# Kernel tuning notes

Hardware: AMD Instinct MI355X
Metric: run time of the kernel (lower is better)

## Reference

```python
import jax, jax.numpy as jnp
import numpy as np

L, H, D_IN, D_OUT = 2, 768, 768, 512


def _gru_layer(x, w_ih, w_hh, b_ih, b_hh):
    # x: [B,T,D]; w_ih: [3H,D]; w_hh: [3H,H]; b_ih,b_hh: [3H]
    # PyTorch GRU gate order: r, z, n
    gates_x = jnp.einsum('btd,gd->btg', x, w_ih) + b_ih  # [B,T,3H], precomputed once
    gates_x = jnp.swapaxes(gates_x, 0, 1)  # [T,B,3H] for scan over time
    h0 = jnp.zeros((x.shape[0], w_hh.shape[1]), dtype=x.dtype)

    def step(h, gx):
        gh = h @ w_hh.T + b_hh  # [B,3H]
        xr, xz, xn = jnp.split(gx, 3, axis=-1)
        hr, hz, hn = jnp.split(gh, 3, axis=-1)
        r = jax.nn.sigmoid(xr + hr)
        z = jax.nn.sigmoid(xz + hz)
        n = jnp.tanh(xn + r * hn)
        h_new = (1.0 - z) * n + z * h
        return h_new, h_new

    _, ys = jax.lax.scan(step, h0, gates_x)  # ys: [T,B,H]
    return jnp.swapaxes(ys, 0, 1)  # [B,T,H]


def setup_inputs() -> dict:
    key = jax.random.key(0)
    ks = jax.random.split(key, 6)
    B, T = 16, 1024
    s = 1.0 / np.sqrt(H)  # PyTorch RNN init scale
    x = jax.random.normal(ks[0], (B, T, D_IN), dtype=jnp.float32)
    # stacked per-layer GRU weights (D_IN == H so layer 0 stacks cleanly)
    w_ih = jax.random.uniform(ks[1], (L, 3 * H, H), minval=-s, maxval=s, dtype=jnp.float32)
    w_hh = jax.random.uniform(ks[2], (L, 3 * H, H), minval=-s, maxval=s, dtype=jnp.float32)
    b_ih = jax.random.uniform(ks[3], (L, 3 * H), minval=-s, maxval=s, dtype=jnp.float32)
    b_hh = jax.random.uniform(ks[4], (L, 3 * H), minval=-s, maxval=s, dtype=jnp.float32)
    w_fc = jax.random.normal(ks[5], (D_OUT, H), dtype=jnp.float32) * 0.02
    b_fc = jnp.zeros((D_OUT,), dtype=jnp.float32)
    return {"x": x, "w_ih": w_ih, "w_hh": w_hh, "b_ih": b_ih, "b_hh": b_hh,
            "w_fc": w_fc, "b_fc": b_fc}


def reference(x, w_ih, w_hh, b_ih, b_hh, w_fc, b_fc):
    out = x
    for l in range(L):  # small fixed layer loop
        out = _gru_layer(out, w_ih[l], w_hh[l], b_ih[l], b_hh[l])
    out = jnp.einsum('bth,oh->bto', out, w_fc) + b_fc  # Linear(768->512)
    return jax.nn.gelu(out, approximate=False)  # torch gelu (exact)
```

## Files before the change

kernel.cpp:

```cpp
#include <hip/hip_runtime.h>
#include <hip/hip_bf16.h>

#define H     768
#define G3    2304
#define BATCH 16
#define TLEN  1024
#define DOUT  512
#define SLICE 32
#define WPG   24
#define NSCAN 96
#define NFC   64
#define NWG   160
#define NTHR  384

typedef __attribute__((ext_vector_type(8))) short short8;
typedef __attribute__((ext_vector_type(4))) float f32x4;
typedef __attribute__((ext_vector_type(4))) unsigned int u32x4;

union U8 { short8 s; unsigned u[4]; unsigned long long q[2]; };

__device__ __forceinline__ float b2f(ushort u) {
  union { unsigned int ui; float f; } v; v.ui = ((unsigned int)u) << 16; return v.f;
}
__device__ __forceinline__ ushort f2b(float f) {
  union { float f; unsigned int ui; } v; v.f = f;
  unsigned int u = v.ui;
  return (ushort)((u + 0x7fffu + ((u >> 16) & 1u)) >> 16);
}

__device__ __forceinline__ unsigned long long agent_ld64(const void* p) {
  return __hip_atomic_load((const unsigned long long*)p, __ATOMIC_RELAXED, __HIP_MEMORY_SCOPE_AGENT);
}
__device__ __forceinline__ unsigned agent_ld32(const void* p) {
  return __hip_atomic_load((const unsigned*)p, __ATOMIC_RELAXED, __HIP_MEMORY_SCOPE_AGENT);
}
__device__ __forceinline__ void agent_st32(void* p, unsigned v) {
  __hip_atomic_store((unsigned*)p, v, __ATOMIC_RELAXED, __HIP_MEMORY_SCOPE_AGENT);
}
__device__ __forceinline__ void agent_st64(void* p, unsigned long long v) {
  __hip_atomic_store((unsigned long long*)p, v, __ATOMIC_RELAXED, __HIP_MEMORY_SCOPE_AGENT);
}

__device__ __forceinline__ void ld64B_agent(const void* p, u32x4* r) {
  asm volatile(
    "global_load_dwordx4 %0, %4, off sc0 sc1\n\t"
    "global_load_dwordx4 %1, %4, off offset:16 sc0 sc1\n\t"
    "global_load_dwordx4 %2, %4, off offset:32 sc0 sc1\n\t"
    "global_load_dwordx4 %3, %4, off offset:48 sc0 sc1\n\t"
    "s_waitcnt vmcnt(0)"
    : "=&v"(r[0]), "=&v"(r[1]), "=&v"(r[2]), "=&v"(r[3])
    : "v"(p) : "memory");
}

__device__ __forceinline__ short8 loadA8(const void* base, bool bf, size_t eidx) {
  if (bf) return *(const short8*)((const ushort*)base + eidx);
  const uint4* f = (const uint4*)((const float*)base + eidx);
  uint4 lo = f[0];
  uint4 hi = f[1];
  U8 r;
  r.u[0] = __builtin_amdgcn_perm(lo.y, lo.x, 0x07060302);
  r.u[1] = __builtin_amdgcn_perm(lo.w, lo.z, 0x07060302);
  r.u[2] = __builtin_amdgcn_perm(hi.y, hi.x, 0x07060302);
  r.u[3] = __builtin_amdgcn_perm(hi.w, hi.z, 0x07060302);
  return r.s;
}
__device__ __forceinline__ short8 loadW8(const void* base, bool bf, size_t eidx) {
  if (bf) return *(const short8*)((const ushort*)base + eidx);
  const float* f = (const float*)base + eidx;
  short8 r;
  #pragma unroll
  for (int i = 0; i < 8; i++) r[i] = (short)f2b(f[i]);
  return r;
}
__device__ __forceinline__ float loadS(const void* p, bool bf, size_t i) {
  return bf ? b2f(((const ushort*)p)[i]) : ((const float*)p)[i];
}

__device__ __forceinline__ bool detect_bf16(const unsigned* xw, int tid, int nthr, int* sh) {
  if (tid == 0) *sh = 0;
  __syncthreads();
  int c = 0;
  for (int i = tid; i < 4096; i += nthr) {
    int e = (int)((xw[i] >> 7) & 0xFF);
    c += (e >= 110 && e <= 140) ? 1 : 0;
  }
  atomicAdd(sh, c);
  __syncthreads();
  return *sh > 2048;
}

__device__ __forceinline__ unsigned* flagp(unsigned* flags, int grp, int wgi, int rep) {
  return flags + (((grp * WPG + wgi) * 4 + rep) * 32);
}

__global__ __launch_bounds__(NTHR) void scan_kernel(
    const void* __restrict__ x,
    const void* __restrict__ w_ih,
    const void* __restrict__ w_hh,
    const void* __restrict__ b_ih,
    const void* __restrict__ b_hh,
    const void* __restrict__ w_fc,
    const void* __restrict__ b_fc,
    unsigned int* flags,
    ushort* h1buf,
    float*  gxbuf1,
    float*  gxbuf2,
    ushort* y2,
    void* __restrict__ out)
{
  const int wg   = blockIdx.x;
  const int tid  = threadIdx.x;
  const int wave = tid >> 6;
  const int lane = tid & 63;
  const int quad = lane >> 4;

  __shared__ ushort h_lds[BATCH * H];
  __shared__ float ghs[96 * 17];
  __shared__ float hold[BATCH * SLICE];
  __shared__ float bih_s[96], bhh_s[96];
  __shared__ int   detsh;

  const bool isbf = detect_bf16((const unsigned*)x, tid, NTHR, &detsh);

  if (wg >= NSCAN) {
    const int fcw = wg - NSCAN;
    const unsigned* fpoll = (wave == 0 && lane < WPG)
        ? flagp(flags, 3, lane, (fcw < 32) ? 2 : 3) : nullptr;
    const int sb  = tid / 24;
    const int seg = tid % 24;
    const int sx  = sb & 7;
    const int ar  = lane & 15;
    const int arx = ar & 7;

    for (int i = 0; i < 16; i++) {
      const int t = fcw + 64 * i;
      if (wave == 0) {
        const int tgt = t + 5;
        for (;;) {
          int v = fpoll ? (int)agent_ld32(fpoll) : 0x7FFFFFFF;
          if (__ballot(v < tgt) == 0ull) break;
          __builtin_amdgcn_s_sleep(8);
        }
      }
      __syncthreads();

      {
        const ushort* src = y2 + ((size_t)sb * TLEN + t) * H + seg * 32;
        u32x4 r4[4];
        ld64B_agent(src, r4);
        #pragma unroll
        for (int j = 0; j < 4; j++)
          *(u32x4*)&h_lds[sb * H + (((seg * 4 + j) ^ sx) * 8)] = r4[j];
      }
      __syncthreads();

      if (wave < 4) {
        const int n0 = wave * 128;
        const ushort* abase = &h_lds[ar * H];
        f32x4 acc[8];
        #pragma unroll
        for (int nt = 0; nt < 8; nt++) acc[nt] = (f32x4){0.f, 0.f, 0.f, 0.f};
        for (int kk = 0; kk < 12; kk++) {
          short8 a0 = *(const short8*)&abase[((quad + 4 * kk) ^ arx) * 8];
          short8 a1 = *(const short8*)&abase[((quad + 4 * (kk + 12)) ^ arx) * 8];
          #pragma unroll
          for (int nt = 0; nt < 8; nt++) {
            const size_t bb = (size_t)(n0 + nt * 16 + ar) * H + quad * 8;
            short8 b0 = loadA8(w_fc, isbf, bb + kk * 32);
            short8 b1 = loadA8(w_fc, isbf, bb + (kk + 12) * 32);
            acc[nt] = __builtin_amdgcn_mfma_f32_16x16x32_bf16(a0, b0, acc[nt], 0, 0, 0);
            acc[nt] = __builtin_amdgcn_mfma_f32_16x16x32_bf16(a1, b1, acc[nt], 0, 0, 0);
          }
        }
        #pragma unroll
        for (int nt = 0; nt < 8; nt++) {
          #pragma unroll
          for (int i2 = 0; i2 < 4; i2++) {
            const int b = quad * 4 + i2;
            const int n = n0 + nt * 16 + ar;
            float v = acc[nt][i2] + loadS(b_fc, isbf, n);
            float g = 0.5f * v * (1.0f + erff(v * 0.70710678118654752f));
            if (isbf) ((ushort*)out)[((size_t)b * TLEN + t) * DOUT + n] = f2b(g);
            else      ((float*)out)[((size_t)b * TLEN + t) * DOUT + n] = g;
          }
        }
      }
      __syncthreads();
    }
    return;
  }

  const int grp  = wg / WPG;
  const int wgi  = wg % WPG;
  const bool isL = (grp == 1 || grp == 3);

  for (int i = tid; i < BATCH * SLICE; i += NTHR) hold[i] = 0.0f;

  if (isL) {
    size_t boff = (grp == 3) ? (size_t)G3 : 0;
    for (int gf = tid; gf < 96; gf += NTHR) {
      size_t gidx = boff + (size_t)(gf >> 5) * H + wgi * SLICE + (gf & 31);
      bih_s[gf] = loadS(b_ih, isbf, gidx);
      bhh_s[gf] = loadS(b_hh, isbf, gidx);
    }
  }

  const unsigned* pollp = nullptr;
  int polloff = 0;
  if (wave == 0) {
    if (grp == 0) {
      if (lane == 0) { pollp = flagp(flags, 1, wgi, 2); polloff = -2; }
    } else if (grp == 1) {
      if      (lane == 0)  { pollp = flagp(flags, 0, wgi, 0);       polloff = 0;  }
      else if (lane <= 24) { pollp = flagp(flags, 1, lane - 1, 0);  polloff = 0;  }
      else if (lane <= 48) { pollp = flagp(flags, 2, lane - 25, 0); polloff = -2; }
    } else if (grp == 2) {
      if      (lane < 24)  { pollp = flagp(flags, 1, lane, 1);      polloff = 0;  }
      else if (lane == 24) { pollp = flagp(flags, 3, wgi, 1);       polloff = -1; }
    } else {
      if      (lane == 0)  { pollp = flagp(flags, 2, wgi, 1);       polloff = -1; }
      else if (lane <= 24) { pollp = flagp(flags, 3, lane - 1, 0);  polloff = 0;  }
    }
  }

  const void* Wmat = (grp == 0 || grp == 2) ? w_ih : w_hh;
  const size_t woff = (grp >= 2) ? (size_t)G3 * H : 0;
  const int gate   = wave >> 1;
  const int gfbase = gate * SLICE + (wave & 1) * 16;
  const int nrow   = gate * H + wgi * SLICE + (wave & 1) * 16 + (lane & 15);
  const size_t wbase = woff + (size_t)nrow * H + quad * 8;

  short8 bfrag[24];
  #pragma unroll
  for (int kk = 0; kk < 24; kk++)
    bfrag[kk] = loadW8(Wmat, isbf, wbase + kk * 32);

  const int sb  = tid / 24;
  const int seg = tid % 24;
  const int sx  = sb & 7;

  const int pb = tid >> 4;
  const int pj = (tid & 15) * 2;
  const bool pact = isL && (tid < BATCH * SLICE / 2);

  const int lag = (grp == 1) ? 1 : ((grp == 2) ? 2 : ((grp == 3) ? 4 : 0));

  __syncthreads();

  for (int t = 0; t < TLEN + 4; t++) {
    const int tau = t - lag;
    const bool active = (tau >= 0) && (tau < TLEN);

    if (active) {
      if (wave == 0) {
        for (;;) {
          int v = pollp ? (int)agent_ld32(pollp) : 0x7FFFFFFF;
          if (__ballot(v < t + polloff) == 0ull) break;
          __builtin_amdgcn_s_sleep(1);
        }
      }
      __syncthreads();

      unsigned long long gr01 = 0, gz01 = 0, gn01 = 0;
      if (pact) {
        const float* gxr = ((grp == 1) ? gxbuf1 : gxbuf2)
            + ((size_t)((tau & 3) * WPG + wgi) * BATCH + pb) * 96;
        gr01 = agent_ld64(gxr + pj);
        gz01 = agent_ld64(gxr + 32 + pj);
        gn01 = agent_ld64(gxr + 64 + pj);
      }

      if (grp == 0) {
        const size_t srcbase = ((size_t)sb * TLEN + tau) * H + seg * 32;
        #pragma unroll
        for (int i = 0; i < 4; i++) {
          short8 v = loadA8(x, isbf, srcbase + i * 8);
          *(short8*)&h_lds[sb * H + (((seg * 4 + i) ^ sx) * 8)] = v;
        }
      } else {
        const int hstep = (grp == 3) ? (t - 5) : (t - 2);
        u32x4 r4[4];
        if (hstep >= 0) {
          const ushort* src = (grp == 3)
              ? y2 + ((size_t)sb * TLEN + hstep) * H + seg * 32
              : h1buf + (size_t)(hstep & 3) * (BATCH * H) + (size_t)sb * H + seg * 32;
          ld64B_agent(src, r4);
        } else {
          r4[0] = (u32x4){0u, 0u, 0u, 0u};
          r4[1] = r4[0]; r4[2] = r4[0]; r4[3] = r4[0];
        }
        #pragma unroll
        for (int j = 0; j < 4; j++)
          *(u32x4*)&h_lds[sb * H + (((seg * 4 + j) ^ sx) * 8)] = r4[j];
      }
      __syncthreads();

      const int ar  = lane & 15;
      const int arx = ar & 7;
      const ushort* abase = &h_lds[ar * H];
      f32x4 acc0 = {0.f, 0.f, 0.f, 0.f}, acc1 = {0.f, 0.f, 0.f, 0.f};
      #pragma unroll
      for (int kk = 0; kk < 12; kk++) {
        short8 a0 = *(const short8*)&abase[((quad + 4 * kk) ^ arx) * 8];
        short8 a1 = *(const short8*)&abase[((quad + 4 * (kk + 12)) ^ arx) * 8];
        acc0 = __builtin_amdgcn_mfma_f32_16x16x32_bf16(a0, bfrag[kk],      acc0, 0, 0, 0);
        acc1 = __builtin_amdgcn_mfma_f32_16x16x32_bf16(a1, bfrag[kk + 12], acc1, 0, 0, 0);
      }
      f32x4 acc = acc0 + acc1;

      #pragma unroll
      for (int i = 0; i < 4; i++)
        ghs[(gfbase + ar) * 17 + quad * 4 + i] = acc[i];
      __syncthreads();

      if (!isL) {
        float* gxout = ((grp == 0) ? gxbuf1 : gxbuf2)
            + ((size_t)(tau & 3) * WPG + wgi) * BATCH * 96;
        const int m  = tid / 24;
        const int c4 = (tid % 24) * 4;
        union { unsigned long long q; float f[2]; } p0, p1;
        p0.f[0] = ghs[(c4 + 0) * 17 + m];
        p0.f[1] = ghs[(c4 + 1) * 17 + m];
        p1.f[0] = ghs[(c4 + 2) * 17 + m];
        p1.f[1] = ghs[(c4 + 3) * 17 + m];
        agent_st64(gxout + (size_t)m * 96 + c4,     p0.q);
        agent_st64(gxout + (size_t)m * 96 + c4 + 2, p1.q);
      } else if (pact) {
        union { unsigned long long q; float f[2]; } ur, uz, un;
        ur.q = gr01; uz.q = gz01; un.q = gn01;
        unsigned hpack = 0;
        #pragma unroll
        for (int s = 0; s < 2; s++) {
          const int j = pj + s;
          float rpre = ur.f[s] + bih_s[j]      + ghs[j * 17 + pb]        + bhh_s[j];
          float zpre = uz.f[s] + bih_s[32 + j] + ghs[(32 + j) * 17 + pb] + bhh_s[32 + j];
          float hn   = ghs[(64 + j) * 17 + pb] + bhh_s[64 + j];
          float r = 1.0f / (1.0f + expf(-rpre));
          float z = 1.0f / (1.0f + expf(-zpre));
          float n = tanhf(un.f[s] + bih_s[64 + j] + r * hn);
          float hnew = (1.0f - z) * n + z * hold[pb * SLICE + j];
          hold[pb * SLICE + j] = hnew;
          hpack |= ((unsigned)f2b(hnew)) << (16 * s);
        }
        if (grp == 1)
          agent_st32(h1buf + (size_t)(tau & 3) * (BATCH * H)
                           + (size_t)pb * H + wgi * SLICE + pj, hpack);
        else
          agent_st32(&y2[((size_t)pb * TLEN + tau) * H + wgi * SLICE + pj], hpack);
      }
    }

    __syncthreads();
    if (tid < 4) agent_st32(flagp(flags, grp, wgi, tid), (unsigned)(t + 1));
  }
}

extern "C" void kernel_launch(void* const* d_in, const int* in_sizes, int n_in,
                              void* d_out, int out_size, void* d_ws, size_t ws_size,
                              hipStream_t stream) {
  const void* x    = d_in[0];
  const void* w_ih = d_in[1];
  const void* w_hh = d_in[2];
  const void* b_ih = d_in[3];
  const void* b_hh = d_in[4];
  const void* w_fc = d_in[5];
  const void* b_fc = d_in[6];

  char* ws = (char*)d_ws;
  unsigned int* flags = (unsigned int*)(ws);
  ushort* h1buf  = (ushort*)(ws + 53248);
  float*  gxbuf1 = (float*)(ws + 151552);
  float*  gxbuf2 = (float*)(ws + 741376);
  ushort* y2     = (ushort*)(ws + 1331200);

  hipMemsetAsync(ws, 0, 49152, stream);
  scan_kernel<<<dim3(NWG), dim3(NTHR), 0, stream>>>(
      x, w_ih, w_hh, b_ih, b_hh, w_fc, b_fc, flags,
      h1buf, gxbuf1, gxbuf2, y2, d_out);
}
```

Measured before the change: 3.553 ms.

## Replace block barriers with per-wave LDS flags and per-chunk flag polling in GRU scan

Changes the A-operand staging in the scan workgroups. Each wave now loads its own K-chunks of the input or hidden state into a new MFMA-friendly LDS layout, and signals readiness through workgroup-scope atomic flags, replacing the two __syncthreads barriers on the step's critical path. Waves poll only the producer flags for the chunks they need, rather than wave 0 polling every producer. The goal is to cut barrier and polling latency in the serial recurrence, at the cost of spin-waiting on LDS atomics and subtler memory-ordering correctness.

```diff
diff --git a/kernel.cpp b/kernel.cpp
--- a/kernel.cpp
+++ b/kernel.cpp
@@ -50,6 +50,19 @@
     "s_waitcnt vmcnt(0)"
     : "=&v"(r[0]), "=&v"(r[1]), "=&v"(r[2]), "=&v"(r[3])
     : "v"(p) : "memory");
+}
+
+__device__ __forceinline__ void ld4x16B_agent(const void* p0, const void* p1,
+                                              const void* p2, const void* p3,
+                                              u32x4* r) {
+  asm volatile(
+    "global_load_dwordx4 %0, %4, off sc0 sc1\n\t"
+    "global_load_dwordx4 %1, %5, off sc0 sc1\n\t"
+    "global_load_dwordx4 %2, %6, off sc0 sc1\n\t"
+    "global_load_dwordx4 %3, %7, off sc0 sc1\n\t"
+    "s_waitcnt vmcnt(0)"
+    : "=&v"(r[0]), "=&v"(r[1]), "=&v"(r[2]), "=&v"(r[3])
+    : "v"(p0), "v"(p1), "v"(p2), "v"(p3) : "memory");
 }
 
 __device__ __forceinline__ short8 loadA8(const void* base, bool bf, size_t eidx) {
@@ -113,12 +126,15 @@
   const int wave = tid >> 6;
   const int lane = tid & 63;
   const int quad = lane >> 4;
-
-  __shared__ ushort h_lds[BATCH * H];
+  const int ar   = lane & 15;
+
+  __shared__ ushort lA[24 * 512];
   __shared__ float ghs[96 * 17];
   __shared__ float hold[BATCH * SLICE];
   __shared__ float bih_s[96], bhh_s[96];
-  __shared__ int   detsh;
+  __shared__ int wready[6];
+  __shared__ int slackok;
+  __shared__ int detsh;
 
   const bool isbf = detect_bf16((const unsigned*)x, tid, NTHR, &detsh);
 
@@ -129,7 +145,6 @@
     const int sb  = tid / 24;
     const int seg = tid % 24;
     const int sx  = sb & 7;
-    const int ar  = lane & 15;
     const int arx = ar & 7;
 
     for (int i = 0; i < 16; i++) {
@@ -150,13 +165,13 @@
         ld64B_agent(src, r4);
         #pragma unroll
         for (int j = 0; j < 4; j++)
-          *(u32x4*)&h_lds[sb * H + (((seg * 4 + j) ^ sx) * 8)] = r4[j];
+          *(u32x4*)&lA[sb * H + (((seg * 4 + j) ^ sx) * 8)] = r4[j];
       }
       __syncthreads();
 
       if (wave < 4) {
         const int n0 = wave * 128;
-        const ushort* abase = &h_lds[ar * H];
+        const ushort* abase = &lA[ar * H];
         f32x4 acc[8];
         #pragma unroll
         for (int nt = 0; nt < 8; nt++) acc[nt] = (f32x4){0.f, 0.f, 0.f, 0.f};
@@ -195,6 +210,8 @@
   const bool isL = (grp == 1 || grp == 3);
 
   for (int i = tid; i < BATCH * SLICE; i += NTHR) hold[i] = 0.0f;
+  if (tid == 0) slackok = -1;
+  if (tid < 6) wready[tid] = -1;
 
   if (isL) {
     size_t boff = (grp == 3) ? (size_t)G3 : 0;
@@ -212,22 +229,26 @@
       if (lane == 0) { pollp = flagp(flags, 1, wgi, 2); polloff = -2; }
     } else if (grp == 1) {
       if      (lane == 0)  { pollp = flagp(flags, 0, wgi, 0);       polloff = 0;  }
-      else if (lane <= 24) { pollp = flagp(flags, 1, lane - 1, 0);  polloff = 0;  }
-      else if (lane <= 48) { pollp = flagp(flags, 2, lane - 25, 0); polloff = -2; }
+      else if (lane <= 24) { pollp = flagp(flags, 2, lane - 1, 0);  polloff = -2; }
     } else if (grp == 2) {
-      if      (lane < 24)  { pollp = flagp(flags, 1, lane, 1);      polloff = 0;  }
-      else if (lane == 24) { pollp = flagp(flags, 3, wgi, 1);       polloff = -1; }
+      if (lane == 0) { pollp = flagp(flags, 3, wgi, 1); polloff = -1; }
     } else {
-      if      (lane == 0)  { pollp = flagp(flags, 2, wgi, 1);       polloff = -1; }
-      else if (lane <= 24) { pollp = flagp(flags, 3, lane - 1, 0);  polloff = 0;  }
+      if (lane == 0) { pollp = flagp(flags, 2, wgi, 1); polloff = -1; }
     }
+  }
+
+  const unsigned* sfl = nullptr;
+  if (grp != 0 && lane < 4) {
+    const int fg = (grp == 3) ? 3 : 1;
+    const int fr = (grp == 2) ? 1 : 0;
+    sfl = flagp(flags, fg, wave + 6 * lane, fr);
   }
 
   const void* Wmat = (grp == 0 || grp == 2) ? w_ih : w_hh;
   const size_t woff = (grp >= 2) ? (size_t)G3 * H : 0;
   const int gate   = wave >> 1;
   const int gfbase = gate * SLICE + (wave & 1) * 16;
-  const int nrow   = gate * H + wgi * SLICE + (wave & 1) * 16 + (lane & 15);
+  const int nrow   = gate * H + wgi * SLICE + (wave & 1) * 16 + ar;
   const size_t wbase = woff + (size_t)nrow * H + quad * 8;
 
   short8 bfrag[24];
@@ -235,10 +256,6 @@
   for (int kk = 0; kk < 24; kk++)
     bfrag[kk] = loadW8(Wmat, isbf, wbase + kk * 32);
 
-  const int sb  = tid / 24;
-  const int seg = tid % 24;
-  const int sx  = sb & 7;
-
   const int pb = tid >> 4;
   const int pj = (tid & 15) * 2;
   const bool pact = isL && (tid < BATCH * SLICE / 2);
@@ -252,14 +269,57 @@
     const bool active = (tau >= 0) && (tau < TLEN);
 
     if (active) {
+      if (grp == 0) {
+        #pragma unroll
+        for (int s = 0; s < 4; s++) {
+          const int kk = wave + 6 * s;
+          short8 v = loadA8(x, isbf,
+              ((size_t)ar * TLEN + tau) * H + kk * 32 + quad * 8);
+          *(short8*)&lA[kk * 512 + ar * 32 + quad * 8] = v;
+        }
+      } else {
+        const int hstep = (grp == 3) ? (t - 5) : (t - 2);
+        if (hstep >= 0) {
+          for (;;) {
+            int v = sfl ? (int)agent_ld32(sfl) : 0x7FFFFFFF;
+            if (__ballot(v < t) == 0ull) break;
+            __builtin_amdgcn_s_sleep(1);
+          }
+          const ushort* srcb = (grp == 3)
+              ? y2 + ((size_t)ar * TLEN + hstep) * H + quad * 8
+              : h1buf + (size_t)(hstep & 3) * (BATCH * H) + (size_t)ar * H + quad * 8;
+          u32x4 r4[4];
+          ld4x16B_agent(srcb + (wave +  0) * 32, srcb + (wave +  6) * 32,
+                        srcb + (wave + 12) * 32, srcb + (wave + 18) * 32, r4);
+          *(u32x4*)&lA[(wave +  0) * 512 + ar * 32 + quad * 8] = r4[0];
+          *(u32x4*)&lA[(wave +  6) * 512 + ar * 32 + quad * 8] = r4[1];
+          *(u32x4*)&lA[(wave + 12) * 512 + ar * 32 + quad * 8] = r4[2];
+          *(u32x4*)&lA[(wave + 18) * 512 + ar * 32 + quad * 8] = r4[3];
+        } else {
+          u32x4 z = (u32x4){0u, 0u, 0u, 0u};
+          #pragma unroll
+          for (int s = 0; s < 4; s++)
+            *(u32x4*)&lA[(wave + 6 * s) * 512 + ar * 32 + quad * 8] = z;
+        }
+      }
+      if (lane == 0)
+        __hip_atomic_store(&wready[wave], t, __ATOMIC_RELEASE,
+                           __HIP_MEMORY_SCOPE_WORKGROUP);
+
       if (wave == 0) {
         for (;;) {
           int v = pollp ? (int)agent_ld32(pollp) : 0x7FFFFFFF;
           if (__ballot(v < t + polloff) == 0ull) break;
           __builtin_amdgcn_s_sleep(1);
         }
-      }
-      __syncthreads();
+        if (lane == 0)
+          __hip_atomic_store(&slackok, t, __ATOMIC_RELEASE,
+                             __HIP_MEMORY_SCOPE_WORKGROUP);
+      } else {
+        while (__hip_atomic_load(&slackok, __ATOMIC_ACQUIRE,
+                                 __HIP_MEMORY_SCOPE_WORKGROUP) < t)
+          __builtin_amdgcn_s_sleep(1);
+      }
 
       unsigned long long gr01 = 0, gz01 = 0, gn01 = 0;
       if (pact) {
@@ -270,39 +330,20 @@
         gn01 = agent_ld64(gxr + 64 + pj);
       }
 
-      if (grp == 0) {
-        const size_t srcbase = ((size_t)sb * TLEN + tau) * H + seg * 32;
-        #pragma unroll
-        for (int i = 0; i < 4; i++) {
-          short8 v = loadA8(x, isbf, srcbase + i * 8);
-          *(short8*)&h_lds[sb * H + (((seg * 4 + i) ^ sx) * 8)] = v;
-        }
-      } else {
-        const int hstep = (grp == 3) ? (t - 5) : (t - 2);
-        u32x4 r4[4];
-        if (hstep >= 0) {
-          const ushort* src = (grp == 3)
-              ? y2 + ((size_t)sb * TLEN + hstep) * H + seg * 32
-              : h1buf + (size_t)(hstep & 3) * (BATCH * H) + (size_t)sb * H + seg * 32;
-          ld64B_agent(src, r4);
-        } else {
-          r4[0] = (u32x4){0u, 0u, 0u, 0u};
-          r4[1] = r4[0]; r4[2] = r4[0]; r4[3] = r4[0];
-        }
-        #pragma unroll
-        for (int j = 0; j < 4; j++)
-          *(u32x4*)&h_lds[sb * H + (((seg * 4 + j) ^ sx) * 8)] = r4[j];
-      }
-      __syncthreads();
-
-      const int ar  = lane & 15;
-      const int arx = ar & 7;
-      const ushort* abase = &h_lds[ar * H];
+      for (;;) {
+        bool ok = true;
+        #pragma unroll
+        for (int w2 = 0; w2 < 6; w2++)
+          ok &= (__hip_atomic_load(&wready[w2], __ATOMIC_ACQUIRE,
+                                   __HIP_MEMORY_SCOPE_WORKGROUP) >= t);
+        if (ok) break;
+      }
+
       f32x4 acc0 = {0.f, 0.f, 0.f, 0.f}, acc1 = {0.f, 0.f, 0.f, 0.f};
       #pragma unroll
       for (int kk = 0; kk < 12; kk++) {
-        short8 a0 = *(const short8*)&abase[((quad + 4 * kk) ^ arx) * 8];
-        short8 a1 = *(const short8*)&abase[((quad + 4 * (kk + 12)) ^ arx) * 8];
+        short8 a0 = *(const short8*)&lA[kk * 512 + ar * 32 + quad * 8];
+        short8 a1 = *(const short8*)&lA[(kk + 12) * 512 + ar * 32 + quad * 8];
         acc0 = __builtin_amdgcn_mfma_f32_16x16x32_bf16(a0, bfrag[kk],      acc0, 0, 0, 0);
         acc1 = __builtin_amdgcn_mfma_f32_16x16x32_bf16(a1, bfrag[kk + 12], acc1, 0, 0, 0);
       }
```

Result: slower. 3.854 ms (+8.5%).
